# Kernel optimization log

Measured on AMD Instinct MI355X. Metric: run time of the kernel, lower is better.

The kernel has to match this reference:

```python
import jax, jax.numpy as jnp
import numpy as np

N_HEADS = 16
EMBED_DIM = 1024
HEAD_DIM = EMBED_DIM // N_HEADS
SEQ_LEN = 2048


def setup_inputs() -> dict:
    key = jax.random.key(0)
    ks = jax.random.split(key, 9)
    s = 1.0 / np.sqrt(EMBED_DIM)
    inp = {
        "x": jax.random.normal(ks[0], (SEQ_LEN, EMBED_DIM), dtype=jnp.float32),
        "Wq": jax.random.uniform(ks[1], (EMBED_DIM, EMBED_DIM), jnp.float32, -s, s),
        "bq": jax.random.uniform(ks[2], (EMBED_DIM,), jnp.float32, -s, s),
        "Wk": jax.random.uniform(ks[3], (EMBED_DIM, EMBED_DIM), jnp.float32, -s, s),
        "bk": jax.random.uniform(ks[4], (EMBED_DIM,), jnp.float32, -s, s),
        "Wv": jax.random.uniform(ks[5], (EMBED_DIM, EMBED_DIM), jnp.float32, -s, s),
        "bv": jax.random.uniform(ks[6], (EMBED_DIM,), jnp.float32, -s, s),
        "Wo": jax.random.uniform(ks[7], (EMBED_DIM, EMBED_DIM), jnp.float32, -s, s),
        "bo": jax.random.uniform(ks[8], (EMBED_DIM,), jnp.float32, -s, s),
    }
    return inp


def reference(x, Wq, bq, Wk, bk, Wv, bv, Wo, bo):
    # Linear layers (torch convention: y = x @ W.T + b)
    Q = x @ Wq.T + bq  # [S, E]
    K = x @ Wk.T + bk
    V = x @ Wv.T + bv
    # split heads -> [H, S, D]
    def split(t):
        return t.reshape(SEQ_LEN, N_HEADS, HEAD_DIM).transpose(1, 0, 2)
    Qh, Kh, Vh = split(Q), split(K), split(V)
    # NOTE: faithful to source, scale is sqrt(embed_dim), not sqrt(head_dim)
    scale = 1.0 / np.sqrt(EMBED_DIM)
    scores = jnp.einsum("hsd,htd->hst", Qh, Kh) * scale  # [H, S, S]
    attn = jax.nn.softmax(scores, axis=-1)
    ctx = jnp.einsum("hst,htd->hsd", attn, Vh)  # [H, S, D]
    ctx = ctx.transpose(1, 0, 2).reshape(SEQ_LEN, EMBED_DIM)
    out = ctx @ Wo.T + bo
    return (out, attn)
```

## Files before the change

### kernel.cpp

```cpp
#include <hip/hip_runtime.h>
#include <hip/hip_bf16.h>

#define SQL 2048
#define EMB 1024
#define NHD 16
#define HDD 64

typedef __bf16 bf16x8 __attribute__((ext_vector_type(8)));
typedef __bf16 bf16x4 __attribute__((ext_vector_type(4)));
typedef float f32x4 __attribute__((ext_vector_type(4)));

__device__ __forceinline__ f32x4 mfma16(bf16x8 a, bf16x8 b, f32x4 c) {
    return __builtin_amdgcn_mfma_f32_16x16x32_bf16(a, b, c, 0, 0, 0);
}

__global__ void cast_bf16_kernel(const float* __restrict__ in, __bf16* __restrict__ out, int n4) {
    int i = blockIdx.x * blockDim.x + threadIdx.x;
    if (i >= n4) return;
    float4 v = ((const float4*)in)[i];
    bf16x4 o;
    o[0] = (__bf16)v.x; o[1] = (__bf16)v.y; o[2] = (__bf16)v.z; o[3] = (__bf16)v.w;
    ((bf16x4*)out)[i] = o;
}

template<bool OUT_BF16>
__global__ __launch_bounds__(256, 2)
void gemm_bt(const __bf16* __restrict__ A,
             const __bf16* __restrict__ B0, const __bf16* __restrict__ B1, const __bf16* __restrict__ B2,
             const float* __restrict__ bias0, const float* __restrict__ bias1, const float* __restrict__ bias2,
             void* __restrict__ out0, void* __restrict__ out1, void* __restrict__ out2,
             int M, int N, int K)
{
    const __bf16* B = B0; const float* bias = bias0; void* Cout = out0;
    if (blockIdx.z == 1) { B = B1; bias = bias1; Cout = out1; }
    if (blockIdx.z == 2) { B = B2; bias = bias2; Cout = out2; }

    __shared__ __attribute__((aligned(16))) __bf16 As[128][40];
    __shared__ __attribute__((aligned(16))) __bf16 Bs[128][40];

    const int tid  = threadIdx.x;
    const int lane = tid & 63;
    const int wave = tid >> 6;
    const int lrow = lane & 15;
    const int quad = lane >> 4;
    const int bm = blockIdx.y * 128;
    const int bn = blockIdx.x * 128;
    const int wm = (wave >> 1) * 64;
    const int wn = (wave & 1) * 64;

    const f32x4 fzero = {0.f, 0.f, 0.f, 0.f};
    f32x4 acc[4][4];
#pragma unroll
    for (int i = 0; i < 4; i++)
#pragma unroll
        for (int j = 0; j < 4; j++) acc[i][j] = fzero;

    for (int k0 = 0; k0 < K; k0 += 32) {
        __syncthreads();
#pragma unroll
        for (int i = 0; i < 2; i++) {
            int lin = tid + i * 256;
            int r  = lin >> 2;
            int cg = (lin & 3) << 3;
            *(bf16x8*)&As[r][cg] = *(const bf16x8*)&A[(size_t)(bm + r) * K + k0 + cg];
            *(bf16x8*)&Bs[r][cg] = *(const bf16x8*)&B[(size_t)(bn + r) * K + k0 + cg];
        }
        __syncthreads();
        bf16x8 af[4], bfr[4];
#pragma unroll
        for (int i = 0; i < 4; i++) af[i]  = *(const bf16x8*)&As[wm + i * 16 + lrow][quad * 8];
#pragma unroll
        for (int i = 0; i < 4; i++) bfr[i] = *(const bf16x8*)&Bs[wn + i * 16 + lrow][quad * 8];
#pragma unroll
        for (int mi = 0; mi < 4; mi++)
#pragma unroll
            for (int ni = 0; ni < 4; ni++)
                acc[mi][ni] = mfma16(af[mi], bfr[ni], acc[mi][ni]);
    }

#pragma unroll
    for (int mi = 0; mi < 4; mi++) {
        int row = bm + wm + mi * 16 + quad * 4;
#pragma unroll
        for (int ni = 0; ni < 4; ni++) {
            int col = bn + wn + ni * 16 + lrow;
            float bv = bias[col];
#pragma unroll
            for (int r = 0; r < 4; r++) {
                float v = acc[mi][ni][r] + bv;
                if (OUT_BF16) ((__bf16*)Cout)[(size_t)(row + r) * N + col] = (__bf16)v;
                else          ((float*)Cout)[(size_t)(row + r) * N + col] = v;
            }
        }
    }
}

__global__ __launch_bounds__(256, 2)
void transpose_v(const __bf16* __restrict__ V, __bf16* __restrict__ Vt) {
    __shared__ __attribute__((aligned(16))) __bf16 tile[64][72];
    const int tid = threadIdx.x;
    const int s0 = blockIdx.x * 64;
    const int c0 = blockIdx.y * 64;
#pragma unroll
    for (int i = 0; i < 2; i++) {
        int lin = tid + i * 256;
        int r  = lin >> 3;
        int cg = (lin & 7) << 3;
        *(bf16x8*)&tile[r][cg] = *(const bf16x8*)&V[(size_t)(s0 + r) * EMB + c0 + cg];
    }
    __syncthreads();
#pragma unroll
    for (int i = 0; i < 2; i++) {
        int lin = tid + i * 256;
        int c  = lin >> 3;
        int sg = (lin & 7) << 3;
        bf16x8 t;
#pragma unroll
        for (int j = 0; j < 8; j++) t[j] = tile[sg + j][c];
        *(bf16x8*)&Vt[(size_t)(c0 + c) * SQL + s0 + sg] = t;
    }
}

__global__ __launch_bounds__(256, 2)
void attn_kernel(const __bf16* __restrict__ Qg, const __bf16* __restrict__ Kg,
                 const __bf16* __restrict__ Vt, float* __restrict__ attn,
                 __bf16* __restrict__ ctx)
{
    __shared__ __attribute__((aligned(16))) __bf16 Ks[64][72];
    __shared__ __attribute__((aligned(16))) __bf16 Vs[64][72];
    __shared__ __attribute__((aligned(16))) __bf16 Ps[4][16][72];

    const int tid  = threadIdx.x;
    const int lane = tid & 63;
    const int w    = tid >> 6;
    const int lrow = lane & 15;
    const int quad = lane >> 4;
    const int h  = blockIdx.y;
    const int q0 = blockIdx.x * 64;
    const float scale = 0.03125f;
    const f32x4 fzero = {0.f, 0.f, 0.f, 0.f};

    const size_t qoff = (size_t)(q0 + w * 16 + lrow) * EMB + h * HDD;
    const bf16x8 qf0 = *(const bf16x8*)&Qg[qoff + quad * 8];
    const bf16x8 qf1 = *(const bf16x8*)&Qg[qoff + 32 + quad * 8];

    float m[4], l[4];
#pragma unroll
    for (int r = 0; r < 4; r++) { m[r] = -1e30f; l[r] = 0.f; }

    for (int k0 = 0; k0 < SQL; k0 += 64) {
        __syncthreads();
#pragma unroll
        for (int i = 0; i < 2; i++) {
            int lin = tid + i * 256;
            int r  = lin >> 3;
            int cg = (lin & 7) << 3;
            *(bf16x8*)&Ks[r][cg] = *(const bf16x8*)&Kg[(size_t)(k0 + r) * EMB + h * HDD + cg];
        }
        __syncthreads();
        f32x4 st[4];
#pragma unroll
        for (int nt = 0; nt < 4; nt++) {
            bf16x8 b0 = *(const bf16x8*)&Ks[nt * 16 + lrow][quad * 8];
            bf16x8 b1 = *(const bf16x8*)&Ks[nt * 16 + lrow][32 + quad * 8];
            f32x4 a = fzero;
            a = mfma16(qf0, b0, a);
            a = mfma16(qf1, b1, a);
            st[nt] = a;
        }
#pragma unroll
        for (int r = 0; r < 4; r++) {
            float tm = fmaxf(fmaxf(st[0][r], st[1][r]), fmaxf(st[2][r], st[3][r])) * scale;
#pragma unroll
            for (int d = 1; d < 16; d <<= 1) tm = fmaxf(tm, __shfl_xor(tm, d));
            float mn = fmaxf(m[r], tm);
            float rs = 0.f;
#pragma unroll
            for (int nt = 0; nt < 4; nt++) rs += __expf(st[nt][r] * scale - mn);
#pragma unroll
            for (int d = 1; d < 16; d <<= 1) rs += __shfl_xor(rs, d);
            l[r] = l[r] * __expf(m[r] - mn) + rs;
            m[r] = mn;
        }
    }

    float rinv[4];
#pragma unroll
    for (int r = 0; r < 4; r++) rinv[r] = 1.f / l[r];

    f32x4 o[4];
#pragma unroll
    for (int nt = 0; nt < 4; nt++) o[nt] = fzero;

    float* attn_h = attn + (size_t)h * SQL * SQL;

    for (int k0 = 0; k0 < SQL; k0 += 64) {
        __syncthreads();
#pragma unroll
        for (int i = 0; i < 2; i++) {
            int lin = tid + i * 256;
            int r  = lin >> 3;
            int cg = (lin & 7) << 3;
            *(bf16x8*)&Ks[r][cg] = *(const bf16x8*)&Kg[(size_t)(k0 + r) * EMB + h * HDD + cg];
            *(bf16x8*)&Vs[r][cg] = *(const bf16x8*)&Vt[(size_t)(h * HDD + r) * SQL + k0 + cg];
        }
        __syncthreads();
#pragma unroll
        for (int nt = 0; nt < 4; nt++) {
            bf16x8 b0 = *(const bf16x8*)&Ks[nt * 16 + lrow][quad * 8];
            bf16x8 b1 = *(const bf16x8*)&Ks[nt * 16 + lrow][32 + quad * 8];
            f32x4 a = fzero;
            a = mfma16(qf0, b0, a);
            a = mfma16(qf1, b1, a);
#pragma unroll
            for (int r = 0; r < 4; r++) {
                float p = __expf(a[r] * scale - m[r]) * rinv[r];
                attn_h[(size_t)(q0 + w * 16 + quad * 4 + r) * SQL + k0 + nt * 16 + lrow] = p;
                Ps[w][quad * 4 + r][nt * 16 + lrow] = (__bf16)p;
            }
        }
        bf16x8 pf0 = *(const bf16x8*)&Ps[w][lrow][quad * 8];
        bf16x8 pf1 = *(const bf16x8*)&Ps[w][lrow][32 + quad * 8];
#pragma unroll
        for (int nt = 0; nt < 4; nt++) {
            bf16x8 v0 = *(const bf16x8*)&Vs[nt * 16 + lrow][quad * 8];
            bf16x8 v1 = *(const bf16x8*)&Vs[nt * 16 + lrow][32 + quad * 8];
            o[nt] = mfma16(pf0, v0, o[nt]);
            o[nt] = mfma16(pf1, v1, o[nt]);
        }
    }

#pragma unroll
    for (int nt = 0; nt < 4; nt++)
#pragma unroll
        for (int r = 0; r < 4; r++)
            ctx[(size_t)(q0 + w * 16 + quad * 4 + r) * EMB + h * HDD + nt * 16 + lrow] = (__bf16)o[nt][r];
}

extern "C" void kernel_launch(void* const* d_in, const int* in_sizes, int n_in,
                              void* d_out, int out_size, void* d_ws, size_t ws_size,
                              hipStream_t stream)
{
    const float* x  = (const float*)d_in[0];
    const float* Wq = (const float*)d_in[1];
    const float* bq = (const float*)d_in[2];
    const float* Wk = (const float*)d_in[3];
    const float* bk = (const float*)d_in[4];
    const float* Wv = (const float*)d_in[5];
    const float* bv = (const float*)d_in[6];
    const float* Wo = (const float*)d_in[7];
    const float* bo = (const float*)d_in[8];

    float* out  = (float*)d_out;
    float* attn = out + (size_t)SQL * EMB;

    const size_t M1 = 1u << 20;
    __bf16* wsb = (__bf16*)d_ws;
    __bf16* xb  = wsb;
    __bf16* wqb = wsb + 2 * M1;
    __bf16* wkb = wsb + 3 * M1;
    __bf16* wvb = wsb + 4 * M1;
    __bf16* wob = wsb + 5 * M1;
    __bf16* Qb  = wsb + 6 * M1;
    __bf16* Kb  = wsb + 8 * M1;
    __bf16* Vb  = wsb + 10 * M1;
    __bf16* Vtb = wsb + 12 * M1;
    __bf16* ctb = wsb + 14 * M1;

    cast_bf16_kernel<<<(SQL * EMB / 4 + 255) / 256, 256, 0, stream>>>(x,  xb,  SQL * EMB / 4);
    cast_bf16_kernel<<<(EMB * EMB / 4 + 255) / 256, 256, 0, stream>>>(Wq, wqb, EMB * EMB / 4);
    cast_bf16_kernel<<<(EMB * EMB / 4 + 255) / 256, 256, 0, stream>>>(Wk, wkb, EMB * EMB / 4);
    cast_bf16_kernel<<<(EMB * EMB / 4 + 255) / 256, 256, 0, stream>>>(Wv, wvb, EMB * EMB / 4);
    cast_bf16_kernel<<<(EMB * EMB / 4 + 255) / 256, 256, 0, stream>>>(Wo, wob, EMB * EMB / 4);

    gemm_bt<true><<<dim3(EMB / 128, SQL / 128, 3), 256, 0, stream>>>(
        xb, wqb, wkb, wvb, bq, bk, bv,
        (void*)Qb, (void*)Kb, (void*)Vb, SQL, EMB, EMB);

    transpose_v<<<dim3(SQL / 64, EMB / 64), 256, 0, stream>>>(Vb, Vtb);

    attn_kernel<<<dim3(SQL / 64, NHD), 256, 0, stream>>>(Qb, Kb, Vtb, attn, ctb);

    gemm_bt<false><<<dim3(EMB / 128, SQL / 128, 1), 256, 0, stream>>>(
        ctb, wob, wob, wob, bo, bo, bo,
        (void*)out, (void*)out, (void*)out, SQL, EMB, EMB);
}
```

Measured before the change: 447.6 us.

## Use direct global-to-LDS loads in GEMM, fold softmax scale into Q, vectorize attn stores

The GEMM now stages A/B tiles with global_load_lds, writing straight into unpadded shared memory instead of going through registers. The softmax scale is folded into the Q projection epilogue. The attention score MFMA operands are swapped so each lane holds 4 consecutive key columns of one query row. That allows vectorized float4 stores of the attention matrix and a cheaper cross-lane max/sum reduction. The costs are possible LDS bank conflicts from dropping the padding, and a slight rounding change from scaling Q before the bf16 cast.

```diff
diff --git a/kernel.cpp b/kernel.cpp
--- a/kernel.cpp
+++ b/kernel.cpp
@@ -1,5 +1,6 @@
 #include <hip/hip_runtime.h>
 #include <hip/hip_bf16.h>
+#include <stdint.h>
 
 #define SQL 2048
 #define EMB 1024
@@ -12,6 +13,13 @@
 
 __device__ __forceinline__ f32x4 mfma16(bf16x8 a, bf16x8 b, f32x4 c) {
     return __builtin_amdgcn_mfma_f32_16x16x32_bf16(a, b, c, 0, 0, 0);
+}
+
+__device__ __forceinline__ void gload_lds16(const __bf16* g, __bf16* lds) {
+    __builtin_amdgcn_global_load_lds(
+        (const __attribute__((address_space(1))) uint32_t*)g,
+        (__attribute__((address_space(3))) uint32_t*)lds,
+        16, 0, 0);
 }
 
 __global__ void cast_bf16_kernel(const float* __restrict__ in, __bf16* __restrict__ out, int n4) {
@@ -29,14 +37,15 @@
              const __bf16* __restrict__ B0, const __bf16* __restrict__ B1, const __bf16* __restrict__ B2,
              const float* __restrict__ bias0, const float* __restrict__ bias1, const float* __restrict__ bias2,
              void* __restrict__ out0, void* __restrict__ out1, void* __restrict__ out2,
+             float s0, float s1, float s2,
              int M, int N, int K)
 {
-    const __bf16* B = B0; const float* bias = bias0; void* Cout = out0;
-    if (blockIdx.z == 1) { B = B1; bias = bias1; Cout = out1; }
-    if (blockIdx.z == 2) { B = B2; bias = bias2; Cout = out2; }
-
-    __shared__ __attribute__((aligned(16))) __bf16 As[128][40];
-    __shared__ __attribute__((aligned(16))) __bf16 Bs[128][40];
+    const __bf16* B = B0; const float* bias = bias0; void* Cout = out0; float cscale = s0;
+    if (blockIdx.z == 1) { B = B1; bias = bias1; Cout = out1; cscale = s1; }
+    if (blockIdx.z == 2) { B = B2; bias = bias2; Cout = out2; cscale = s2; }
+
+    __shared__ __attribute__((aligned(16))) __bf16 As[128 * 32];
+    __shared__ __attribute__((aligned(16))) __bf16 Bs[128 * 32];
 
     const int tid  = threadIdx.x;
     const int lane = tid & 63;
@@ -55,22 +64,23 @@
 #pragma unroll
         for (int j = 0; j < 4; j++) acc[i][j] = fzero;
 
+    const int srow = (lane >> 2);
+    const int scol = (lane & 3) * 8;
+
     for (int k0 = 0; k0 < K; k0 += 32) {
         __syncthreads();
 #pragma unroll
         for (int i = 0; i < 2; i++) {
-            int lin = tid + i * 256;
-            int r  = lin >> 2;
-            int cg = (lin & 3) << 3;
-            *(bf16x8*)&As[r][cg] = *(const bf16x8*)&A[(size_t)(bm + r) * K + k0 + cg];
-            *(bf16x8*)&Bs[r][cg] = *(const bf16x8*)&B[(size_t)(bn + r) * K + k0 + cg];
+            int rbase = wave * 32 + i * 16;
+            gload_lds16(&A[(size_t)(bm + rbase + srow) * K + k0 + scol], &As[rbase * 32]);
+            gload_lds16(&B[(size_t)(bn + rbase + srow) * K + k0 + scol], &Bs[rbase * 32]);
         }
         __syncthreads();
         bf16x8 af[4], bfr[4];
 #pragma unroll
-        for (int i = 0; i < 4; i++) af[i]  = *(const bf16x8*)&As[wm + i * 16 + lrow][quad * 8];
-#pragma unroll
-        for (int i = 0; i < 4; i++) bfr[i] = *(const bf16x8*)&Bs[wn + i * 16 + lrow][quad * 8];
+        for (int i = 0; i < 4; i++) af[i]  = *(const bf16x8*)&As[(wm + i * 16 + lrow) * 32 + quad * 8];
+#pragma unroll
+        for (int i = 0; i < 4; i++) bfr[i] = *(const bf16x8*)&Bs[(wn + i * 16 + lrow) * 32 + quad * 8];
 #pragma unroll
         for (int mi = 0; mi < 4; mi++)
 #pragma unroll
@@ -87,7 +97,7 @@
             float bv = bias[col];
 #pragma unroll
             for (int r = 0; r < 4; r++) {
-                float v = acc[mi][ni][r] + bv;
+                float v = (acc[mi][ni][r] + bv) * cscale;
                 if (OUT_BF16) ((__bf16*)Cout)[(size_t)(row + r) * N + col] = (__bf16)v;
                 else          ((float*)Cout)[(size_t)(row + r) * N + col] = v;
             }
@@ -137,16 +147,13 @@
     const int quad = lane >> 4;
     const int h  = blockIdx.y;
     const int q0 = blockIdx.x * 64;
-    const float scale = 0.03125f;
     const f32x4 fzero = {0.f, 0.f, 0.f, 0.f};
 
     const size_t qoff = (size_t)(q0 + w * 16 + lrow) * EMB + h * HDD;
     const bf16x8 qf0 = *(const bf16x8*)&Qg[qoff + quad * 8];
     const bf16x8 qf1 = *(const bf16x8*)&Qg[qoff + 32 + quad * 8];
 
-    float m[4], l[4];
-#pragma unroll
-    for (int r = 0; r < 4; r++) { m[r] = -1e30f; l[r] = 0.f; }
+    float m = -1e30f, l = 0.f;
 
     for (int k0 = 0; k0 < SQL; k0 += 64) {
         __syncthreads();
@@ -163,36 +170,36 @@
         for (int nt = 0; nt < 4; nt++) {
             bf16x8 b0 = *(const bf16x8*)&Ks[nt * 16 + lrow][quad * 8];
             bf16x8 b1 = *(const bf16x8*)&Ks[nt * 16 + lrow][32 + quad * 8];
-            f32x4 a = fzero;
-            a = mfma16(qf0, b0, a);
-            a = mfma16(qf1, b1, a);
+            f32x4 a = mfma16(b0, qf0, fzero);
+            a = mfma16(b1, qf1, a);
             st[nt] = a;
         }
-#pragma unroll
-        for (int r = 0; r < 4; r++) {
-            float tm = fmaxf(fmaxf(st[0][r], st[1][r]), fmaxf(st[2][r], st[3][r])) * scale;
-#pragma unroll
-            for (int d = 1; d < 16; d <<= 1) tm = fmaxf(tm, __shfl_xor(tm, d));
-            float mn = fmaxf(m[r], tm);
-            float rs = 0.f;
-#pragma unroll
-            for (int nt = 0; nt < 4; nt++) rs += __expf(st[nt][r] * scale - mn);
-#pragma unroll
-            for (int d = 1; d < 16; d <<= 1) rs += __shfl_xor(rs, d);
-            l[r] = l[r] * __expf(m[r] - mn) + rs;
-            m[r] = mn;
-        }
-    }
-
-    float rinv[4];
-#pragma unroll
-    for (int r = 0; r < 4; r++) rinv[r] = 1.f / l[r];
+        float tm = -1e30f;
+#pragma unroll
+        for (int nt = 0; nt < 4; nt++)
+#pragma unroll
+            for (int r = 0; r < 4; r++) tm = fmaxf(tm, st[nt][r]);
+        tm = fmaxf(tm, __shfl_xor(tm, 16));
+        tm = fmaxf(tm, __shfl_xor(tm, 32));
+        float mn = fmaxf(m, tm);
+        float rs = 0.f;
+#pragma unroll
+        for (int nt = 0; nt < 4; nt++)
+#pragma unroll
+            for (int r = 0; r < 4; r++) rs += __expf(st[nt][r] - mn);
+        rs += __shfl_xor(rs, 16);
+        rs += __shfl_xor(rs, 32);
+        l = l * __expf(m - mn) + rs;
+        m = mn;
+    }
+
+    const float rinv = 1.f / l;
 
     f32x4 o[4];
 #pragma unroll
     for (int nt = 0; nt < 4; nt++) o[nt] = fzero;
 
-    float* attn_h = attn + (size_t)h * SQL * SQL;
+    float* __restrict__ arow = attn + (size_t)h * SQL * SQL + (size_t)(q0 + w * 16 + lrow) * SQL;
 
     for (int k0 = 0; k0 < SQL; k0 += 64) {
         __syncthreads();
@@ -209,15 +216,18 @@
         for (int nt = 0; nt < 4; nt++) {
             bf16x8 b0 = *(const bf16x8*)&Ks[nt * 16 + lrow][quad * 8];
             bf16x8 b1 = *(const bf16x8*)&Ks[nt * 16 + lrow][32 + quad * 8];
-            f32x4 a = fzero;
-            a = mfma16(qf0, b0, a);
-            a = mfma16(qf1, b1, a);
+            f32x4 a = mfma16(b0, qf0, fzero);
+            a = mfma16(b1, qf1, a);
+            f32x4 pv;
+            bf16x4 pb;
 #pragma unroll
             for (int r = 0; r < 4; r++) {
-                float p = __expf(a[r] * scale - m[r]) * rinv[r];
-                attn_h[(size_t)(q0 + w * 16 + quad * 4 + r) * SQL + k0 + nt * 16 + lrow] = p;
-                Ps[w][quad * 4 + r][nt * 16 + lrow] = (__bf16)p;
+                float p = __expf(a[r] - m) * rinv;
+                pv[r] = p;
+                pb[r] = (__bf16)p;
             }
+            *(f32x4*)&arow[k0 + nt * 16 + quad * 4] = pv;
+            *(bf16x4*)&Ps[w][lrow][nt * 16 + quad * 4] = pb;
         }
         bf16x8 pf0 = *(const bf16x8*)&Ps[w][lrow][quad * 8];
         bf16x8 pf1 = *(const bf16x8*)&Ps[w][lrow][32 + quad * 8];
@@ -275,7 +285,8 @@
 
     gemm_bt<true><<<dim3(EMB / 128, SQL / 128, 3), 256, 0, stream>>>(
         xb, wqb, wkb, wvb, bq, bk, bv,
-        (void*)Qb, (void*)Kb, (void*)Vb, SQL, EMB, EMB);
+        (void*)Qb, (void*)Kb, (void*)Vb,
+        0.03125f, 1.0f, 1.0f, SQL, EMB, EMB);
 
     transpose_v<<<dim3(SQL / 64, EMB / 64), 256, 0, stream>>>(Vb, Vtb);
 
@@ -283,5 +294,6 @@
 
     gemm_bt<false><<<dim3(EMB / 128, SQL / 128, 1), 256, 0, stream>>>(
         ctb, wob, wob, wob, bo, bo, bo,
-        (void*)out, (void*)out, (void*)out, SQL, EMB, EMB);
-}
+        (void*)out, (void*)out, (void*)out,
+        1.0f, 1.0f, 1.0f, SQL, EMB, EMB);
+}
```

Result: faster. 409.5 us (-8.5%).
